# Optimization experiments

Measured on AMD Instinct MI355X. Metric: run time of the kernel, lower is better.

The kernel has to match this reference:

```python
import jax, jax.numpy as jnp
import numpy as np

B, N, E = 2, 2048, 1024   # batch, seq_len, embed_dim (= hidden_dim)
H, HD = 16, 64            # num_heads, head_dim


def setup_inputs() -> dict:
    key = jax.random.key(0)
    ks = jax.random.split(key, 6)
    w = lambda k: jax.random.normal(k, (E, E), jnp.float32) * 0.02
    return {
        "x": jax.random.normal(ks[0], (B, N, E), jnp.float32),
        "Wq": w(ks[1]), "bq": jnp.zeros((E,), jnp.float32),
        "Wk": w(ks[2]), "bk": jnp.zeros((E,), jnp.float32),
        "Wv": w(ks[3]), "bv": jnp.zeros((E,), jnp.float32),
        "Wu": w(ks[4]), "bu": jnp.zeros((E,), jnp.float32),
        "Wo": w(ks[5]), "bo": jnp.zeros((E,), jnp.float32),
        "ln_g": jnp.ones((E,), jnp.float32),
        "ln_b": jnp.zeros((E,), jnp.float32),
    }


def reference(x, Wq, bq, Wk, bk, Wv, bv, Wu, bu, Wo, bo, ln_g, ln_b):
    # projections (torch Linear: x @ W.T + b)
    q = x @ Wq.T + bq
    k = x @ Wk.T + bk
    v = jax.nn.silu(x @ Wv.T + bv)   # uv_act = swish
    u = jax.nn.silu(x @ Wu.T + bu)
    # split heads: [B, N, H*HD] -> [B, H, N, HD]
    split = lambda t: t.reshape(B, N, H, HD).transpose(0, 2, 1, 3)
    q, k, v = split(q), split(k), split(v)
    # non-softmax attention: ReLU on scaled energy (no causal mask)
    energy = jnp.einsum("bhnd,bhmd->bhnm", q, k) / jnp.float32(np.sqrt(HD))
    energy = jax.nn.relu(energy)
    out = jnp.einsum("bhnm,bhmd->bhnd", energy, v)
    # merge heads: [B, H, N, HD] -> [B, N, H*HD]
    out = out.transpose(0, 2, 1, 3).reshape(B, N, H * HD)
    # layernorm over hidden_dim
    mu = out.mean(-1, keepdims=True)
    var = out.var(-1, keepdims=True)
    out = (out - mu) * jax.lax.rsqrt(var + 1e-5) * ln_g + ln_b
    # gate and output projection
    out = u * out
    return out @ Wo.T + bo
```

## Files before the change

kernel.cpp:

```cpp
#include <hip/hip_runtime.h>
#include <stdint.h>

typedef unsigned short u16;
typedef __attribute__((ext_vector_type(8))) short short8;
typedef __attribute__((ext_vector_type(4))) short short4v;
typedef __attribute__((ext_vector_type(4))) float floatx4;
typedef __attribute__((ext_vector_type(4))) int intx4;

#define B_ 2
#define N_ 2048
#define E_ 1024
#define H_ 16
#define HD_ 64
#define M_TOT (B_ * N_)

__device__ __forceinline__ float bf2f(u16 h) {
    union { unsigned u; float f; } c; c.u = ((unsigned)h) << 16; return c.f;
}
__device__ __forceinline__ u16 f2bf(float f) {
    union { float f; unsigned u; } c; c.f = f;
    unsigned r = c.u + 0x7FFFu + ((c.u >> 16) & 1u);
    return (u16)(r >> 16);
}
__device__ __forceinline__ float silu_f(float x) { return x / (1.f + __expf(-x)); }

template <typename T> __device__ __forceinline__ void store_out(T* p, float v);
template <> __device__ __forceinline__ void store_out<u16>(u16* p, float v)    { *p = f2bf(v); }
template <> __device__ __forceinline__ void store_out<float>(float* p, float v) { *p = v; }

__device__ __forceinline__ void gll16(const void* g, void* l) {
    __builtin_amdgcn_global_load_lds(
        (const __attribute__((address_space(1))) void*)g,
        (__attribute__((address_space(3))) void*)l,
        16, 0, 0);
}

__device__ __forceinline__ short4v relu_pack(floatx4 s) {
    union { float f; unsigned u; } c0, c1, c2, c3;
    c0.f = fmaxf(s[0], 0.f); c1.f = fmaxf(s[1], 0.f);
    c2.f = fmaxf(s[2], 0.f); c3.f = fmaxf(s[3], 0.f);
    unsigned lo = __builtin_amdgcn_perm(c1.u + 0x8000u, c0.u + 0x8000u, 0x07060302);
    unsigned hi = __builtin_amdgcn_perm(c3.u + 0x8000u, c2.u + 0x8000u, 0x07060302);
    union { unsigned v[2]; short4v s4; } r; r.v[0] = lo; r.v[1] = hi;
    return r.s4;
}

__launch_bounds__(256, 4)
__global__ void cvt6(const float* __restrict__ s0, const float* __restrict__ s1,
                     const float* __restrict__ s2, const float* __restrict__ s3,
                     const float* __restrict__ s4, const float* __restrict__ s5,
                     u16* __restrict__ d0, u16* __restrict__ d1,
                     u16* __restrict__ d2, u16* __restrict__ d3,
                     u16* __restrict__ d4, u16* __restrict__ d5)
{
    const int z = blockIdx.z;
    if (z > 0 && blockIdx.x >= E_ * E_ / 2048) return;
    const float* src = (z == 0) ? s0 : (z == 1) ? s1 : (z == 2) ? s2
                     : (z == 3) ? s3 : (z == 4) ? s4 : s5;
    u16* dst         = (z == 0) ? d0 : (z == 1) ? d1 : (z == 2) ? d2
                     : (z == 3) ? d3 : (z == 4) ? d4 : d5;
    const int i = (blockIdx.x * 256 + threadIdx.x) * 8;
    floatx4 a = *(const floatx4*)(src + i);
    floatx4 b = *(const floatx4*)(src + i + 4);
    union { u16 h[8]; intx4 v; } o;
    o.h[0] = f2bf(a[0]); o.h[1] = f2bf(a[1]); o.h[2] = f2bf(a[2]); o.h[3] = f2bf(a[3]);
    o.h[4] = f2bf(b[0]); o.h[5] = f2bf(b[1]); o.h[6] = f2bf(b[2]); o.h[7] = f2bf(b[3]);
    *(intx4*)(dst + i) = o.v;
}

template <typename OutT>
__launch_bounds__(256, 2)
__global__ void gemm4(const u16* __restrict__ A,
                      const u16* __restrict__ W0, const u16* __restrict__ W1,
                      const u16* __restrict__ W2, const u16* __restrict__ W3,
                      const float* __restrict__ bi0, const float* __restrict__ bi1,
                      const float* __restrict__ bi2, const float* __restrict__ bi3,
                      OutT* __restrict__ O0, OutT* __restrict__ O1,
                      OutT* __restrict__ O2, OutT* __restrict__ O3,
                      int actmask, int scalemask, int K)
{
    __shared__ u16 a_lds[128 * 32];
    __shared__ u16 b_lds[128 * 32];

    const int z = blockIdx.z;
    const u16* W    = (z == 0) ? W0 : (z == 1) ? W1 : (z == 2) ? W2 : W3;
    const float* Bi = (z == 0) ? bi0 : (z == 1) ? bi1 : (z == 2) ? bi2 : bi3;
    OutT* Out       = (z == 0) ? O0 : (z == 1) ? O1 : (z == 2) ? O2 : O3;
    const bool act = (actmask >> z) & 1;
    const float osc = ((scalemask >> z) & 1) ? 0.125f : 1.0f;

    const int t    = threadIdx.x;
    const int wave = t >> 6, lane = t & 63, quad = lane >> 4, l16 = lane & 15;
    const int wm = wave >> 1, wn = wave & 1;
    const int m0 = blockIdx.y * 128;
    const int n0 = blockIdx.x * 128;

    floatx4 acc[4][4];
    const floatx4 fz = {0.f, 0.f, 0.f, 0.f};
    for (int i = 0; i < 4; i++)
        for (int j = 0; j < 4; j++) acc[i][j] = fz;

    const int ar = t >> 2;
    const int ac = (t & 3) * 8;
    const u16* Ag0 = A + (size_t)(m0 + ar) * K + ac;
    const u16* Ag1 = A + (size_t)(m0 + 64 + ar) * K + ac;
    const u16* Bg0 = W + (size_t)(n0 + ar) * K + ac;
    const u16* Bg1 = W + (size_t)(n0 + 64 + ar) * K + ac;
    u16* al0 = a_lds + wave * 512;
    u16* al1 = a_lds + 2048 + wave * 512;
    u16* bl0 = b_lds + wave * 512;
    u16* bl1 = b_lds + 2048 + wave * 512;

    for (int k0 = 0; k0 < K; k0 += 32) {
        __syncthreads();
        gll16(Ag0 + k0, al0);
        gll16(Ag1 + k0, al1);
        gll16(Bg0 + k0, bl0);
        gll16(Bg1 + k0, bl1);
        __syncthreads();

        short8 af[4], bfr[4];
        for (int i = 0; i < 4; i++)
            af[i]  = *(const short8*)&a_lds[(wm * 64 + i * 16 + l16) * 32 + quad * 8];
        for (int j = 0; j < 4; j++)
            bfr[j] = *(const short8*)&b_lds[(wn * 64 + j * 16 + l16) * 32 + quad * 8];
        for (int i = 0; i < 4; i++)
            for (int j = 0; j < 4; j++)
                acc[i][j] = __builtin_amdgcn_mfma_f32_16x16x32_bf16(af[i], bfr[j], acc[i][j], 0, 0, 0);
    }

    float bias_v[4];
    for (int j = 0; j < 4; j++) bias_v[j] = Bi[n0 + wn * 64 + j * 16 + l16];

    for (int i = 0; i < 4; i++) {
        const int row = m0 + wm * 64 + i * 16 + quad * 4;
        for (int j = 0; j < 4; j++) {
            const int col = n0 + wn * 64 + j * 16 + l16;
            for (int r = 0; r < 4; r++) {
                float v = acc[i][j][r] + bias_v[j];
                if (act) v = silu_f(v);
                v *= osc;
                store_out<OutT>(&Out[(size_t)(row + r) * E_ + col], v);
            }
        }
    }
}

__launch_bounds__(256, 4)
__global__ void vtrans(const u16* __restrict__ V, u16* __restrict__ VT)
{
    __shared__ u16 ts[64 * 72];
    const int bh = blockIdx.y;
    const int b = bh >> 4, h = bh & 15;
    const int n0 = blockIdx.x * 64;
    const int t = threadIdx.x;
    const int r = t >> 2, seg = (t & 3) * 16;

    const u16* src = V + ((size_t)b * N_ + n0 + r) * E_ + h * HD_ + seg;
    intx4 x0 = *(const intx4*)(src);
    intx4 x1 = *(const intx4*)(src + 8);
    *(intx4*)&ts[r * 72 + seg]     = x0;
    *(intx4*)&ts[r * 72 + seg + 8] = x1;
    __syncthreads();

    union { u16 h[16]; intx4 v[2]; } buf;
    for (int j = 0; j < 16; j++) buf.h[j] = ts[(seg + j) * 72 + r];
    u16* dst = VT + ((size_t)bh * HD_ + r) * N_ + n0 + seg;
    *(intx4*)(dst)     = buf.v[0];
    *(intx4*)(dst + 8) = buf.v[1];
}

#define LK 72
#define KSPLIT 4
#define KCHUNK (N_ / KSPLIT)

__launch_bounds__(256, 2)
__global__ void attn(const u16* __restrict__ Q, const u16* __restrict__ Kk,
                     const u16* __restrict__ VT,
                     u16* __restrict__ P0, u16* __restrict__ P1,
                     u16* __restrict__ P2, u16* __restrict__ P3)
{
    __shared__ u16 k_lds[64 * LK];
    __shared__ u16 v_lds[64 * 64];

    const int bh = blockIdx.y;
    const int b = bh >> 4, h = bh & 15;
    const int z = blockIdx.z;
    u16* __restrict__ Oa = (z == 0) ? P0 : (z == 1) ? P1 : (z == 2) ? P2 : P3;
    const int key_base = z * KCHUNK;

    const int t = threadIdx.x;
    const int wave = t >> 6, lane = t & 63, quad = lane >> 4, l16 = lane & 15;
    const int q0 = blockIdx.x * 256 + wave * 64;
    const size_t base = (size_t)b * N_ * E_ + h * HD_;

    short8 aq[4][2];
    for (int mi = 0; mi < 4; mi++)
        for (int ks = 0; ks < 2; ks++)
            aq[mi][ks] = *(const short8*)(Q + base + (size_t)(q0 + mi * 16 + l16) * E_ + ks * 32 + quad * 8);

    floatx4 o[4][4];
    const floatx4 fz = {0.f, 0.f, 0.f, 0.f};
    for (int mi = 0; mi < 4; mi++)
        for (int nd = 0; nd < 4; nd++) o[mi][nd] = fz;

    const int srow = t >> 2, sseg = (t & 3) * 16;
    const int prow = (srow & 32) + (((srow >> 2) & 1) << 4)
                   + (((srow >> 3) & 3) << 2) + (srow & 3);
    const u16* Ksrc = Kk + base + (size_t)(key_base + srow) * E_ + sseg;
    u16* kdst = &k_lds[prow * LK + sseg];

    const int vd0 = wave * 8 + (lane >> 3);
    const int vk0 = (lane & 7) * 8;
    const u16* Vsrc0 = VT + ((size_t)bh * HD_ + vd0) * N_ + key_base + vk0;
    const u16* Vsrc1 = VT + ((size_t)bh * HD_ + vd0 + 32) * N_ + key_base + vk0;
    u16* vdst0 = v_lds + wave * 512;
    u16* vdst1 = v_lds + 2048 + wave * 512;

    for (int kt = 0; kt < KCHUNK / 64; kt++) {
        __syncthreads();
        const size_t kof = (size_t)(kt * 64) * E_;
        gll16(Vsrc0 + kt * 64, vdst0);
        gll16(Vsrc1 + kt * 64, vdst1);
        intx4 k0v = *(const intx4*)(Ksrc + kof);
        intx4 k1v = *(const intx4*)(Ksrc + kof + 8);
        *(intx4*)(kdst)     = k0v;
        *(intx4*)(kdst + 8) = k1v;
        __syncthreads();

        for (int g = 0; g < 2; g++) {
            short8 ka[2][2];
            for (int tp = 0; tp < 2; tp++)
                for (int ks = 0; ks < 2; ks++)
                    ka[tp][ks] = *(const short8*)&k_lds[(g * 32 + tp * 16 + l16) * LK + ks * 32 + quad * 8];
            short8 bv[4];
            for (int nd = 0; nd < 4; nd++)
                bv[nd] = *(const short8*)&v_lds[(nd * 16 + l16) * 64 + g * 32 + quad * 8];

            for (int mi = 0; mi < 4; mi++) {
                floatx4 c0 = __builtin_amdgcn_mfma_f32_16x16x32_bf16(ka[0][0], aq[mi][0], fz, 0, 0, 0);
                c0 = __builtin_amdgcn_mfma_f32_16x16x32_bf16(ka[0][1], aq[mi][1], c0, 0, 0, 0);
                floatx4 c1 = __builtin_amdgcn_mfma_f32_16x16x32_bf16(ka[1][0], aq[mi][0], fz, 0, 0, 0);
                c1 = __builtin_amdgcn_mfma_f32_16x16x32_bf16(ka[1][1], aq[mi][1], c1, 0, 0, 0);
                union { short4v h[2]; short8 s8; } sf;
                sf.h[0] = relu_pack(c0);
                sf.h[1] = relu_pack(c1);
                for (int nd = 0; nd < 4; nd++)
                    o[mi][nd] = __builtin_amdgcn_mfma_f32_16x16x32_bf16(sf.s8, bv[nd], o[mi][nd], 0, 0, 0);
            }
        }
    }

    for (int mi = 0; mi < 4; mi++)
        for (int nd = 0; nd < 4; nd++)
            for (int r = 0; r < 4; r++)
                Oa[(size_t)(b * N_ + q0 + mi * 16 + quad * 4 + r) * E_ + h * HD_ + nd * 16 + l16] =
                    f2bf(o[mi][nd][r]);
}

__launch_bounds__(256, 4)
__global__ void ln_gate(const u16* __restrict__ P0, const u16* __restrict__ P1,
                        const u16* __restrict__ P2, const u16* __restrict__ P3,
                        const u16* __restrict__ U,
                        const float* __restrict__ G, const float* __restrict__ Bb,
                        u16* __restrict__ Out)
{
    const int row = blockIdx.x;
    const int t = threadIdx.x;
    const size_t idx = (size_t)row * E_ + t * 4;
    const short4v a0 = *(const short4v*)(P0 + idx);
    const short4v a1 = *(const short4v*)(P1 + idx);
    const short4v a2 = *(const short4v*)(P2 + idx);
    const short4v a3 = *(const short4v*)(P3 + idx);
    floatx4 v;
    for (int i = 0; i < 4; i++)
        v[i] = bf2f((u16)a0[i]) + bf2f((u16)a1[i]) + bf2f((u16)a2[i]) + bf2f((u16)a3[i]);
    float s  = v[0] + v[1] + v[2] + v[3];
    float ss = v[0] * v[0] + v[1] * v[1] + v[2] * v[2] + v[3] * v[3];
    for (int off = 32; off; off >>= 1) {
        s  += __shfl_down(s, off, 64);
        ss += __shfl_down(ss, off, 64);
    }
    __shared__ float red[8];
    const int wave = t >> 6, lane = t & 63;
    if (lane == 0) { red[wave] = s; red[4 + wave] = ss; }
    __syncthreads();
    const float S  = red[0] + red[1] + red[2] + red[3];
    const float SS = red[4] + red[5] + red[6] + red[7];
    const float mu  = S * (1.f / E_);
    const float var = SS * (1.f / E_) - mu * mu;
    const float rstd = rsqrtf(var + 1e-5f);

    short4v outv;
    for (int i = 0; i < 4; i++) {
        const int e = t * 4 + i;
        float y = (v[i] - mu) * rstd * G[e] + Bb[e];
        y *= bf2f(U[idx + i]);
        outv[i] = (short)f2bf(y);
    }
    *(short4v*)(Out + idx) = outv;
}

extern "C" void kernel_launch(void* const* d_in, const int* in_sizes, int n_in,
                              void* d_out, int out_size, void* d_ws, size_t ws_size,
                              hipStream_t stream)
{
    const float* x   = (const float*)d_in[0];
    const float* Wq  = (const float*)d_in[1];
    const float* bq  = (const float*)d_in[2];
    const float* Wk  = (const float*)d_in[3];
    const float* bk  = (const float*)d_in[4];
    const float* Wv  = (const float*)d_in[5];
    const float* bv  = (const float*)d_in[6];
    const float* Wu  = (const float*)d_in[7];
    const float* bu  = (const float*)d_in[8];
    const float* Wo  = (const float*)d_in[9];
    const float* bo  = (const float*)d_in[10];
    const float* lng = (const float*)d_in[11];
    const float* lnb = (const float*)d_in[12];

    char* ws = (char*)d_ws;
    u16*  qw  = (u16*)(ws);
    u16*  kw  = (u16*)(ws + 8388608);
    u16*  vw  = (u16*)(ws + 16777216);
    u16*  uw  = (u16*)(ws + 25165824);
    u16*  p0  = (u16*)(ws + 33554432);
    u16*  p1  = (u16*)(ws + 41943040);
    u16*  xb  = (u16*)(ws + 50331648);
    u16*  vt  = (u16*)(ws + 50331648);
    u16*  wbq = (u16*)(ws + 58720256);
    u16*  wbk = (u16*)(ws + 60817408);
    u16*  wbv = (u16*)(ws + 62914560);
    u16*  wbu = (u16*)(ws + 65011712);
    u16*  wbo = (u16*)(ws + 67108864);
    u16*  gw  = (u16*)(ws);

    float* out = (float*)d_out;
    u16*  p2  = (u16*)d_out;
    u16*  p3  = (u16*)d_out + 4194304;

    const dim3 blk(256, 1, 1);

    cvt6<<<dim3(M_TOT * E_ / 2048, 1, 6), blk, 0, stream>>>(
        x, Wq, Wk, Wv, Wu, Wo, xb, wbq, wbk, wbv, wbu, wbo);
    gemm4<u16><<<dim3(8, 32, 4), blk, 0, stream>>>(xb, wbq, wbk, wbv, wbu,
                                                   bq, bk, bv, bu,
                                                   qw, kw, vw, uw, 0xC, 0x1, E_);
    vtrans<<<dim3(N_ / 64, B_ * H_, 1), blk, 0, stream>>>(vw, vt);
    attn<<<dim3(N_ / 256, B_ * H_, KSPLIT), blk, 0, stream>>>(qw, kw, vt, p0, p1, p2, p3);
    ln_gate<<<dim3(M_TOT, 1, 1), blk, 0, stream>>>(p0, p1, p2, p3, uw, lng, lnb, gw);
    gemm4<float><<<dim3(8, 32, 1), blk, 0, stream>>>(gw, wbo, wbo, wbo, wbo,
                                                     bo, bo, bo, bo,
                                                     out, out, out, out, 0x0, 0x0, E_);
}
```

Before: 228.2 us.

## Share A tile across two projection weights per block and pad V LDS tile

The QKVU projection is now one kernel where each block computes two weight matrices against the same A tile. This halves A tile loads and the grid z-dimension, at the cost of double the accumulator registers (128 floats per thread) and extra LDS. In attention, V is now loaded through registers into a padded (stride 72) LDS tile instead of direct global-to-LDS loads, which is meant to reduce bank conflicts on the B-fragment reads. The output GEMM is simplified to a single-weight signature.

```diff
diff --git a/kernel.cpp b/kernel.cpp
--- a/kernel.cpp
+++ b/kernel.cpp
@@ -68,26 +68,106 @@
     *(intx4*)(dst + i) = o.v;
 }
 
+__launch_bounds__(256, 2)
+__global__ void gemm2z(const u16* __restrict__ A,
+                       const u16* __restrict__ W0, const u16* __restrict__ W1,
+                       const u16* __restrict__ W2, const u16* __restrict__ W3,
+                       const float* __restrict__ bi0, const float* __restrict__ bi1,
+                       const float* __restrict__ bi2, const float* __restrict__ bi3,
+                       u16* __restrict__ O0, u16* __restrict__ O1,
+                       u16* __restrict__ O2, u16* __restrict__ O3,
+                       int actmask, int scalemask, int K)
+{
+    __shared__ u16 a_lds[4096];
+    __shared__ u16 b_lds[2][4096];
+
+    const int z = blockIdx.z;
+    const u16* Wa    = (z == 0) ? W0 : W2;
+    const u16* Wb    = (z == 0) ? W1 : W3;
+    const float* Bia = (z == 0) ? bi0 : bi2;
+    const float* Bib = (z == 0) ? bi1 : bi3;
+    u16* Oa          = (z == 0) ? O0 : O2;
+    u16* Ob          = (z == 0) ? O1 : O3;
+
+    const int t    = threadIdx.x;
+    const int wave = t >> 6, lane = t & 63, quad = lane >> 4, l16 = lane & 15;
+    const int wm = wave >> 1, wn = wave & 1;
+    const int m0 = blockIdx.y * 128;
+    const int n0 = blockIdx.x * 128;
+
+    floatx4 acc[2][4][4];
+    const floatx4 fz = {0.f, 0.f, 0.f, 0.f};
+    for (int zz = 0; zz < 2; zz++)
+        for (int i = 0; i < 4; i++)
+            for (int j = 0; j < 4; j++) acc[zz][i][j] = fz;
+
+    const int ar = t >> 2;
+    const int ac = (t & 3) * 8;
+    const u16* Ag0  = A  + (size_t)(m0 + ar) * K + ac;
+    const u16* Ag1  = A  + (size_t)(m0 + 64 + ar) * K + ac;
+    const u16* Bag0 = Wa + (size_t)(n0 + ar) * K + ac;
+    const u16* Bag1 = Wa + (size_t)(n0 + 64 + ar) * K + ac;
+    const u16* Bbg0 = Wb + (size_t)(n0 + ar) * K + ac;
+    const u16* Bbg1 = Wb + (size_t)(n0 + 64 + ar) * K + ac;
+    u16* al0  = a_lds + wave * 512;
+    u16* al1  = a_lds + 2048 + wave * 512;
+    u16* bl00 = b_lds[0] + wave * 512;
+    u16* bl01 = b_lds[0] + 2048 + wave * 512;
+    u16* bl10 = b_lds[1] + wave * 512;
+    u16* bl11 = b_lds[1] + 2048 + wave * 512;
+
+    for (int k0 = 0; k0 < K; k0 += 32) {
+        __syncthreads();
+        gll16(Ag0 + k0, al0);
+        gll16(Ag1 + k0, al1);
+        gll16(Bag0 + k0, bl00);
+        gll16(Bag1 + k0, bl01);
+        gll16(Bbg0 + k0, bl10);
+        gll16(Bbg1 + k0, bl11);
+        __syncthreads();
+
+        short8 af[4];
+        for (int i = 0; i < 4; i++)
+            af[i] = *(const short8*)&a_lds[(wm * 64 + i * 16 + l16) * 32 + quad * 8];
+        for (int zz = 0; zz < 2; zz++) {
+            short8 bfr[4];
+            for (int j = 0; j < 4; j++)
+                bfr[j] = *(const short8*)&b_lds[zz][(wn * 64 + j * 16 + l16) * 32 + quad * 8];
+            for (int i = 0; i < 4; i++)
+                for (int j = 0; j < 4; j++)
+                    acc[zz][i][j] = __builtin_amdgcn_mfma_f32_16x16x32_bf16(af[i], bfr[j], acc[zz][i][j], 0, 0, 0);
+        }
+    }
+
+    for (int zz = 0; zz < 2; zz++) {
+        const float* Bi = zz ? Bib : Bia;
+        u16* Out        = zz ? Ob : Oa;
+        const bool act  = (actmask >> (z * 2 + zz)) & 1;
+        const float osc = ((scalemask >> (z * 2 + zz)) & 1) ? 0.125f : 1.0f;
+        float bias_v[4];
+        for (int j = 0; j < 4; j++) bias_v[j] = Bi[n0 + wn * 64 + j * 16 + l16];
+        for (int i = 0; i < 4; i++) {
+            const int row = m0 + wm * 64 + i * 16 + quad * 4;
+            for (int j = 0; j < 4; j++) {
+                const int col = n0 + wn * 64 + j * 16 + l16;
+                for (int r = 0; r < 4; r++) {
+                    float v = acc[zz][i][j][r] + bias_v[j];
+                    if (act) v = silu_f(v);
+                    v *= osc;
+                    Out[(size_t)(row + r) * E_ + col] = f2bf(v);
+                }
+            }
+        }
+    }
+}
+
 template <typename OutT>
 __launch_bounds__(256, 2)
-__global__ void gemm4(const u16* __restrict__ A,
-                      const u16* __restrict__ W0, const u16* __restrict__ W1,
-                      const u16* __restrict__ W2, const u16* __restrict__ W3,
-                      const float* __restrict__ bi0, const float* __restrict__ bi1,
-                      const float* __restrict__ bi2, const float* __restrict__ bi3,
-                      OutT* __restrict__ O0, OutT* __restrict__ O1,
-                      OutT* __restrict__ O2, OutT* __restrict__ O3,
-                      int actmask, int scalemask, int K)
+__global__ void gemm4(const u16* __restrict__ A, const u16* __restrict__ W,
+                      const float* __restrict__ Bi, OutT* __restrict__ Out, int K)
 {
     __shared__ u16 a_lds[128 * 32];
     __shared__ u16 b_lds[128 * 32];
-
-    const int z = blockIdx.z;
-    const u16* W    = (z == 0) ? W0 : (z == 1) ? W1 : (z == 2) ? W2 : W3;
-    const float* Bi = (z == 0) ? bi0 : (z == 1) ? bi1 : (z == 2) ? bi2 : bi3;
-    OutT* Out       = (z == 0) ? O0 : (z == 1) ? O1 : (z == 2) ? O2 : O3;
-    const bool act = (actmask >> z) & 1;
-    const float osc = ((scalemask >> z) & 1) ? 0.125f : 1.0f;
 
     const int t    = threadIdx.x;
     const int wave = t >> 6, lane = t & 63, quad = lane >> 4, l16 = lane & 15;
@@ -136,12 +216,8 @@
         const int row = m0 + wm * 64 + i * 16 + quad * 4;
         for (int j = 0; j < 4; j++) {
             const int col = n0 + wn * 64 + j * 16 + l16;
-            for (int r = 0; r < 4; r++) {
-                float v = acc[i][j][r] + bias_v[j];
-                if (act) v = silu_f(v);
-                v *= osc;
-                store_out<OutT>(&Out[(size_t)(row + r) * E_ + col], v);
-            }
+            for (int r = 0; r < 4; r++)
+                store_out<OutT>(&Out[(size_t)(row + r) * E_ + col], acc[i][j][r] + bias_v[j]);
         }
     }
 }
@@ -171,6 +247,7 @@
 }
 
 #define LK 72
+#define LV 72
 #define KSPLIT 4
 #define KCHUNK (N_ / KSPLIT)
 
@@ -181,7 +258,7 @@
                      u16* __restrict__ P2, u16* __restrict__ P3)
 {
     __shared__ u16 k_lds[64 * LK];
-    __shared__ u16 v_lds[64 * 64];
+    __shared__ u16 v_lds[64 * LV];
 
     const int bh = blockIdx.y;
     const int b = bh >> 4, h = bh & 15;
@@ -210,22 +287,21 @@
     const u16* Ksrc = Kk + base + (size_t)(key_base + srow) * E_ + sseg;
     u16* kdst = &k_lds[prow * LK + sseg];
 
-    const int vd0 = wave * 8 + (lane >> 3);
-    const int vk0 = (lane & 7) * 8;
-    const u16* Vsrc0 = VT + ((size_t)bh * HD_ + vd0) * N_ + key_base + vk0;
-    const u16* Vsrc1 = VT + ((size_t)bh * HD_ + vd0 + 32) * N_ + key_base + vk0;
-    u16* vdst0 = v_lds + wave * 512;
-    u16* vdst1 = v_lds + 2048 + wave * 512;
+    const u16* Vsrc = VT + ((size_t)bh * HD_ + srow) * N_ + key_base + sseg;
+    u16* vdst = &v_lds[srow * LV + sseg];
 
     for (int kt = 0; kt < KCHUNK / 64; kt++) {
         __syncthreads();
-        const size_t kof = (size_t)(kt * 64) * E_;
-        gll16(Vsrc0 + kt * 64, vdst0);
-        gll16(Vsrc1 + kt * 64, vdst1);
-        intx4 k0v = *(const intx4*)(Ksrc + kof);
-        intx4 k1v = *(const intx4*)(Ksrc + kof + 8);
-        *(intx4*)(kdst)     = k0v;
-        *(intx4*)(kdst + 8) = k1v;
+        const u16* kg = Ksrc + (size_t)(kt * 64) * E_;
+        const u16* vg = Vsrc + kt * 64;
+        intx4 kv0 = *(const intx4*)(kg);
+        intx4 kv1 = *(const intx4*)(kg + 8);
+        intx4 vv0 = *(const intx4*)(vg);
+        intx4 vv1 = *(const intx4*)(vg + 8);
+        *(intx4*)(kdst)     = kv0;
+        *(intx4*)(kdst + 8) = kv1;
+        *(intx4*)(vdst)     = vv0;
+        *(intx4*)(vdst + 8) = vv1;
         __syncthreads();
 
         for (int g = 0; g < 2; g++) {
@@ -235,7 +311,7 @@
                     ka[tp][ks] = *(const short8*)&k_lds[(g * 32 + tp * 16 + l16) * LK + ks * 32 + quad * 8];
             short8 bv[4];
             for (int nd = 0; nd < 4; nd++)
-                bv[nd] = *(const short8*)&v_lds[(nd * 16 + l16) * 64 + g * 32 + quad * 8];
+                bv[nd] = *(const short8*)&v_lds[(nd * 16 + l16) * LV + g * 32 + quad * 8];
 
             for (int mi = 0; mi < 4; mi++) {
                 floatx4 c0 = __builtin_amdgcn_mfma_f32_16x16x32_bf16(ka[0][0], aq[mi][0], fz, 0, 0, 0);
@@ -343,13 +419,11 @@
 
     cvt6<<<dim3(M_TOT * E_ / 2048, 1, 6), blk, 0, stream>>>(
         x, Wq, Wk, Wv, Wu, Wo, xb, wbq, wbk, wbv, wbu, wbo);
-    gemm4<u16><<<dim3(8, 32, 4), blk, 0, stream>>>(xb, wbq, wbk, wbv, wbu,
-                                                   bq, bk, bv, bu,
-                                                   qw, kw, vw, uw, 0xC, 0x1, E_);
+    gemm2z<<<dim3(8, 32, 2), blk, 0, stream>>>(xb, wbq, wbk, wbv, wbu,
+                                               bq, bk, bv, bu,
+                                               qw, kw, vw, uw, 0xC, 0x1, E_);
     vtrans<<<dim3(N_ / 64, B_ * H_, 1), blk, 0, stream>>>(vw, vt);
     attn<<<dim3(N_ / 256, B_ * H_, KSPLIT), blk, 0, stream>>>(qw, kw, vt, p0, p1, p2, p3);
     ln_gate<<<dim3(M_TOT, 1, 1), blk, 0, stream>>>(p0, p1, p2, p3, uw, lng, lnb, gw);
-    gemm4<float><<<dim3(8, 32, 1), blk, 0, stream>>>(gw, wbo, wbo, wbo, wbo,
-                                                     bo, bo, bo, bo,
-                                                     out, out, out, out, 0x0, 0x0, E_);
-}
+    gemm4<float><<<dim3(8, 32, 1), blk, 0, stream>>>(gw, wbo, bo, out, E_);
+}
```

New measurement: 230.3 us. Within noise of the previous version (+0.9%).
